# Performance work log

Measured on AMD Instinct MI355X. Metric: run time of the kernel, lower is better.

## Reference

```python
import jax, jax.numpy as jnp
import numpy as np

D = 1024


def setup_inputs() -> dict:
    key = jax.random.key(0)
    kx, kq, kk, kv, ko = jax.random.split(key, 5)
    scale = 0.02
    x = jax.random.normal(kx, (4, 2048, D), dtype=jnp.float32)
    Wq = jax.random.normal(kq, (D, D), dtype=jnp.float32) * scale
    Wk = jax.random.normal(kk, (D, D), dtype=jnp.float32) * scale
    Wv = jax.random.normal(kv, (D, D), dtype=jnp.float32) * scale
    Wo = jax.random.normal(ko, (D, D), dtype=jnp.float32) * scale
    return {"x": x, "Wq": Wq, "Wk": Wk, "Wv": Wv, "Wo": Wo}


def reference(x, Wq, Wk, Wv, Wo):
    # Linear projections (torch Linear: y = x @ W.T, no bias)
    q = jnp.einsum('bsd,ed->bse', x, Wq)
    k = jnp.einsum('bsd,ed->bse', x, Wk)
    v = jnp.einsum('bsd,ed->bse', x, Wv)
    d = x.shape[-1]
    # HRR binding: circular convolution of k and v along feature dim (rfft domain)
    Fk = jnp.fft.rfft(k, axis=-1)
    Fv = jnp.fft.rfft(v, axis=-1)
    Fq = jnp.fft.rfft(q, axis=-1)
    Fkv = Fk * Fv                      # bound key-value pairs, Fourier domain
    # causal cumulative memory over sequence; FFT is linear so cumsum commutes
    Fmem = jnp.cumsum(Fkv, axis=-2)    # [b, s, d//2+1] complex
    # unbind with query: circular correlation = multiply by conj(rfft(q))
    values_hat = jnp.fft.irfft(Fmem * jnp.conj(Fq), n=d, axis=-1)
    return jnp.einsum('bsd,ed->bse', values_hat, Wo)
```

## Files before the change

kernel.cpp:

```cpp
#include <hip/hip_runtime.h>

#define D_DIM 1024
#define NF 513
#define NB 4
#define NS 2048
#define NTOK (NB * NS)
#define NCH 32
#define CHS (NS / NCH)

typedef __attribute__((ext_vector_type(8))) short short8_t;
typedef __attribute__((ext_vector_type(4))) float f32x4;

__device__ inline unsigned short f2bf(float f) {
    unsigned u = __builtin_bit_cast(unsigned, f);
    u += 0x7FFFu + ((u >> 16) & 1u);
    return (unsigned short)(u >> 16);
}
__device__ inline float bf2f(unsigned short h) {
    unsigned u = ((unsigned)h) << 16;
    return __builtin_bit_cast(float, u);
}
__device__ inline unsigned pkc(float re, float im) {
    return (unsigned)f2bf(re) | ((unsigned)f2bf(im) << 16);
}
__device__ inline float2 upc(unsigned u) {
    return make_float2(bf2f((unsigned short)(u & 0xFFFFu)), bf2f((unsigned short)(u >> 16)));
}

__global__ __launch_bounds__(256) void convert_x(const float* __restrict__ src,
                                                 unsigned short* __restrict__ dst,
                                                 int n4) {
    int i = blockIdx.x * 256 + threadIdx.x;
    int stride = gridDim.x * 256;
    for (; i < n4; i += stride) {
        float4 v = reinterpret_cast<const float4*>(src)[i];
        ushort4 o;
        o.x = f2bf(v.x); o.y = f2bf(v.y); o.z = f2bf(v.z); o.w = f2bf(v.w);
        reinterpret_cast<ushort4*>(dst)[i] = o;
    }
}

__global__ __launch_bounds__(256) void convert_w(const float* __restrict__ Wq,
                                                 const float* __restrict__ Wk,
                                                 const float* __restrict__ Wv,
                                                 const float* __restrict__ Wo,
                                                 unsigned short* __restrict__ Wqkv,
                                                 unsigned short* __restrict__ Wob) {
    int y = blockIdx.y;
    const float* src = (y == 0) ? Wq : (y == 1) ? Wk : (y == 2) ? Wv : Wo;
    unsigned short* dst = (y < 3) ? (Wqkv + (size_t)y * 1048576) : Wob;
    int i = blockIdx.x * 256 + threadIdx.x;
    float4 v = reinterpret_cast<const float4*>(src)[i];
    ushort4 o;
    o.x = f2bf(v.x); o.y = f2bf(v.y); o.z = f2bf(v.z); o.w = f2bf(v.w);
    reinterpret_cast<ushort4*>(dst)[i] = o;
}

__device__ inline void gload_lds16(const void* g, void* l) {
    __builtin_amdgcn_global_load_lds(
        (const __attribute__((address_space(1))) void*)g,
        (__attribute__((address_space(3))) void*)l,
        16, 0, 0);
}

template <typename OutT>
__global__ __launch_bounds__(256) void gemm_bf16_bk64(const unsigned short* __restrict__ A,
                                                      const unsigned short* __restrict__ B,
                                                      OutT* __restrict__ C,
                                                      int M, int N, int K) {
    __shared__ __attribute__((aligned(16))) unsigned short ldsA[2 * 128 * 64];
    __shared__ __attribute__((aligned(16))) unsigned short ldsB[2 * 128 * 64];
    const int tid  = threadIdx.x;
    const int wave = tid >> 6;
    const int lane = tid & 63;
    const int l15  = lane & 15;
    const int q4   = (lane >> 4) & 3;
    const int h7   = l15 & 7;
    const int p0   = ((q4)     ^ h7) << 3;
    const int p1   = ((4 + q4) ^ h7) << 3;
    const int wm   = (wave >> 1) * 64;
    const int wn   = (wave & 1) * 64;
    const int bm   = blockIdx.x * 128;
    const int bn   = blockIdx.y * 128;
    const int srow = tid >> 3;
    const int scol = (((tid & 7) ^ ((tid >> 3) & 7)) << 3);
    const int NT   = K >> 6;

    const unsigned short* Asrc = A + (size_t)(bm + srow) * K + scol;
    const unsigned short* Bsrc = B + (size_t)(bn + srow) * K + scol;
    const size_t cstep = (size_t)32 * K;

    f32x4 acc[4][4];
#pragma unroll
    for (int i = 0; i < 4; ++i)
#pragma unroll
        for (int j = 0; j < 4; ++j)
            acc[i][j] = (f32x4){0.f, 0.f, 0.f, 0.f};

    auto STAGE = [&](int t, int b) {
        const int k0 = t << 6;
        unsigned short* la = &ldsA[b * 8192 + tid * 8];
        unsigned short* lb = &ldsB[b * 8192 + tid * 8];
        gload_lds16(Asrc + k0,             la);
        gload_lds16(Asrc + cstep + k0,     la + 2048);
        gload_lds16(Asrc + 2 * cstep + k0, la + 4096);
        gload_lds16(Asrc + 3 * cstep + k0, la + 6144);
        gload_lds16(Bsrc + k0,             lb);
        gload_lds16(Bsrc + cstep + k0,     lb + 2048);
        gload_lds16(Bsrc + 2 * cstep + k0, lb + 4096);
        gload_lds16(Bsrc + 3 * cstep + k0, lb + 6144);
    };

    STAGE(0, 0);

    for (int j = 0; j < NT; ++j) {
        const int buf = j & 1;
        if (j + 1 < NT) {
            STAGE(j + 1, buf ^ 1);
            asm volatile("s_waitcnt vmcnt(8)" ::: "memory");
        } else {
            asm volatile("s_waitcnt vmcnt(0)" ::: "memory");
        }
        __builtin_amdgcn_s_barrier();
        asm volatile("" ::: "memory");

        const unsigned short* la = &ldsA[buf * 8192];
        const unsigned short* lb = &ldsB[buf * 8192];

        {
            short8_t af[4], bfv[4];
#pragma unroll
            for (int mi = 0; mi < 4; ++mi)
                af[mi] = *reinterpret_cast<const short8_t*>(&la[(wm + mi * 16 + l15) * 64 + p0]);
#pragma unroll
            for (int ni = 0; ni < 4; ++ni)
                bfv[ni] = *reinterpret_cast<const short8_t*>(&lb[(wn + ni * 16 + l15) * 64 + p0]);
            __builtin_amdgcn_s_setprio(1);
#pragma unroll
            for (int mi = 0; mi < 4; ++mi)
#pragma unroll
                for (int ni = 0; ni < 4; ++ni)
                    acc[mi][ni] = __builtin_amdgcn_mfma_f32_16x16x32_bf16(af[mi], bfv[ni], acc[mi][ni], 0, 0, 0);
            __builtin_amdgcn_s_setprio(0);
        }
        {
            short8_t af[4], bfv[4];
#pragma unroll
            for (int mi = 0; mi < 4; ++mi)
                af[mi] = *reinterpret_cast<const short8_t*>(&la[(wm + mi * 16 + l15) * 64 + p1]);
#pragma unroll
            for (int ni = 0; ni < 4; ++ni)
                bfv[ni] = *reinterpret_cast<const short8_t*>(&lb[(wn + ni * 16 + l15) * 64 + p1]);
            __builtin_amdgcn_s_setprio(1);
#pragma unroll
            for (int mi = 0; mi < 4; ++mi)
#pragma unroll
                for (int ni = 0; ni < 4; ++ni)
                    acc[mi][ni] = __builtin_amdgcn_mfma_f32_16x16x32_bf16(af[mi], bfv[ni], acc[mi][ni], 0, 0, 0);
            __builtin_amdgcn_s_setprio(0);
        }

        __builtin_amdgcn_s_barrier();
        asm volatile("" ::: "memory");
    }

#pragma unroll
    for (int mi = 0; mi < 4; ++mi) {
        int rbase = bm + wm + mi * 16 + (lane >> 4) * 4;
#pragma unroll
        for (int ni = 0; ni < 4; ++ni) {
            int col = bn + wn + ni * 16 + l15;
#pragma unroll
            for (int j = 0; j < 4; ++j) {
                float v = acc[mi][ni][j];
                if constexpr (sizeof(OutT) == 4)
                    C[(size_t)(rbase + j) * N + col] = v;
                else
                    C[(size_t)(rbase + j) * N + col] = f2bf(v);
            }
        }
    }
}

__device__ inline int sw(int i) { return i ^ ((i >> 4) & 15); }

__device__ inline int dr4(int n) {
    return ((n & 3) << 8) | (((n >> 2) & 3) << 6) | (((n >> 4) & 3) << 4) |
           (((n >> 6) & 3) << 2) | ((n >> 8) & 3);
}

__device__ inline float2 cmul(float2 a, float2 b) {
    return make_float2(a.x * b.x - a.y * b.y, a.x * b.y + a.y * b.x);
}

__device__ inline void fft1024_r4(float2* X, const float2* tw, int t) {
#pragma unroll
    for (int s = 0; s < 5; ++s) {
        const int L = 1 << (2 * s);
        const int r = t & (L - 1);
        const int base = ((t >> (2 * s)) << (2 * s + 2)) + r;
        float2 A  = X[sw(base)];
        float2 Bv = X[sw(base + L)];
        float2 Cv = X[sw(base + 2 * L)];
        float2 Dv = X[sw(base + 3 * L)];
        if (s != 0) {
            const int step = 1024 >> (2 * s + 2);
            Bv = cmul(Bv, tw[sw(r * step)]);
            Cv = cmul(Cv, tw[sw(2 * r * step)]);
            Dv = cmul(Dv, tw[sw(3 * r * step)]);
        }
        float2 e0 = make_float2(A.x + Cv.x, A.y + Cv.y);
        float2 e1 = make_float2(A.x - Cv.x, A.y - Cv.y);
        float2 o0 = make_float2(Bv.x + Dv.x, Bv.y + Dv.y);
        float2 o1 = make_float2(Bv.x - Dv.x, Bv.y - Dv.y);
        X[sw(base)]         = make_float2(e0.x + o0.x, e0.y + o0.y);
        X[sw(base + L)]     = make_float2(e1.x + o1.y, e1.y - o1.x);
        X[sw(base + 2 * L)] = make_float2(e0.x - o0.x, e0.y - o0.y);
        X[sw(base + 3 * L)] = make_float2(e1.x - o1.y, e1.y + o1.x);
        __syncthreads();
    }
}

__global__ __launch_bounds__(256) void twiddle_init(float2* __restrict__ twg) {
    int k = blockIdx.x * 256 + threadIdx.x;
    if (k < 768) {
        float ang = -6.283185307179586f * (float)k / 1024.0f;
        float s, c;
        sincosf(ang, &s, &c);
        twg[sw(k)] = make_float2(c, s);
    }
}

__global__ __launch_bounds__(256) void hrr_fft_fwd(const unsigned short* __restrict__ QKV,
                                                   const float2* __restrict__ twg,
                                                   unsigned* __restrict__ Fkv,
                                                   unsigned* __restrict__ Fq) {
    __shared__ __attribute__((aligned(16))) float2 X[1024];
    __shared__ __attribute__((aligned(16))) float2 twL[768];
    const int tid = threadIdx.x;
    const int t0 = blockIdx.x * 2, t1 = t0 + 1;
    for (int i = tid; i < 384; i += 256)
        reinterpret_cast<float4*>(twL)[i] = reinterpret_cast<const float4*>(twg)[i];

#pragma unroll
    for (int which = 0; which < 2; ++which) {
        const int tok = which ? t1 : t0;
        const ushort4* Kr = (const ushort4*)(QKV + (size_t)tok * 3072 + 1024);
        const ushort4* Vr = (const ushort4*)(QKV + (size_t)tok * 3072 + 2048);
        ushort4 k4 = Kr[tid], v4 = Vr[tid];
        X[sw(dr4(4 * tid + 0))] = make_float2(bf2f(k4.x), bf2f(v4.x));
        X[sw(dr4(4 * tid + 1))] = make_float2(bf2f(k4.y), bf2f(v4.y));
        X[sw(dr4(4 * tid + 2))] = make_float2(bf2f(k4.z), bf2f(v4.z));
        X[sw(dr4(4 * tid + 3))] = make_float2(bf2f(k4.w), bf2f(v4.w));
        __syncthreads();
        fft1024_r4(X, twL, tid);
        for (int j = tid; j < NF; j += 256) {
            float2 Zj = X[sw(j)];
            float2 Zm = X[sw((1024 - j) & 1023)];
            float2 Fk = make_float2(0.5f * (Zj.x + Zm.x), 0.5f * (Zj.y - Zm.y));
            float2 Fv = make_float2(0.5f * (Zj.y + Zm.y), 0.5f * (Zm.x - Zj.x));
            float2 p = cmul(Fk, Fv);
            Fkv[(size_t)tok * NF + j] = pkc(p.x, p.y);
        }
        __syncthreads();
    }
    {
        const ushort4* Q0 = (const ushort4*)(QKV + (size_t)t0 * 3072);
        const ushort4* Q1 = (const ushort4*)(QKV + (size_t)t1 * 3072);
        ushort4 a4 = Q0[tid], b4 = Q1[tid];
        X[sw(dr4(4 * tid + 0))] = make_float2(bf2f(a4.x), bf2f(b4.x));
        X[sw(dr4(4 * tid + 1))] = make_float2(bf2f(a4.y), bf2f(b4.y));
        X[sw(dr4(4 * tid + 2))] = make_float2(bf2f(a4.z), bf2f(b4.z));
        X[sw(dr4(4 * tid + 3))] = make_float2(bf2f(a4.w), bf2f(b4.w));
        __syncthreads();
        fft1024_r4(X, twL, tid);
        for (int j = tid; j < NF; j += 256) {
            float2 Zj = X[sw(j)];
            float2 Zm = X[sw((1024 - j) & 1023)];
            Fq[(size_t)t0 * NF + j] = pkc(0.5f * (Zj.x + Zm.x), 0.5f * (Zj.y - Zm.y));
            Fq[(size_t)t1 * NF + j] = pkc(0.5f * (Zj.y + Zm.y), 0.5f * (Zm.x - Zj.x));
        }
    }
}

__global__ __launch_bounds__(256) void hrr_chunk_sum(const unsigned* __restrict__ Fkv,
                                                     float2* __restrict__ part) {
    int f = blockIdx.x * 256 + threadIdx.x;
    if (f >= NF) return;
    int ch = blockIdx.y, b = blockIdx.z;
    float sx = 0.f, sy = 0.f;
    size_t base = ((size_t)b * NS + (size_t)ch * CHS) * NF + f;
    for (int i = 0; i < CHS; ++i) {
        float2 t = upc(Fkv[base + (size_t)i * NF]);
        sx += t.x; sy += t.y;
    }
    part[(size_t)(b * NCH + ch) * NF + f] = make_float2(sx, sy);
}

__global__ __launch_bounds__(256) void hrr_scan_apply(unsigned* __restrict__ Fkv,
                                                      const unsigned* __restrict__ Fq,
                                                      const float2* __restrict__ part) {
    int f = blockIdx.x * 256 + threadIdx.x;
    if (f >= NF) return;
    int ch = blockIdx.y, b = blockIdx.z;
    float rx = 0.f, ry = 0.f;
    for (int c2 = 0; c2 < ch; ++c2) {
        float2 p = part[(size_t)(b * NCH + c2) * NF + f];
        rx += p.x; ry += p.y;
    }
    size_t base = ((size_t)b * NS + (size_t)ch * CHS) * NF + f;
    for (int i = 0; i < CHS; ++i) {
        size_t idx = base + (size_t)i * NF;
        float2 kv = upc(Fkv[idx]);
        rx += kv.x; ry += kv.y;
        float2 q = upc(Fq[idx]);
        Fkv[idx] = pkc(rx * q.x + ry * q.y, ry * q.x - rx * q.y);
    }
}

__global__ __launch_bounds__(256) void hrr_ifft(const unsigned* __restrict__ U,
                                                const float2* __restrict__ twg,
                                                unsigned short* __restrict__ vhat) {
    __shared__ __attribute__((aligned(16))) float2 X[1024];
    __shared__ __attribute__((aligned(16))) float2 twL[768];
    const int tid = threadIdx.x;
    const int t0 = blockIdx.x * 2, t1 = t0 + 1;
    for (int i = tid; i < 384; i += 256)
        reinterpret_cast<float4*>(twL)[i] = reinterpret_cast<const float4*>(twg)[i];
    const unsigned* U1 = U + (size_t)t0 * NF;
    const unsigned* U2 = U + (size_t)t1 * NF;
#pragma unroll
    for (int c = 0; c < 4; ++c) {
        int j = tid + (c << 8);
        float2 Cv;
        if (j <= 512) {
            float2 u1 = upc(U1[j]), u2 = upc(U2[j]);
            Cv = make_float2(u1.x - u2.y, -u1.y - u2.x);
        } else {
            int m = 1024 - j;
            float2 u1 = upc(U1[m]), u2 = upc(U2[m]);
            Cv = make_float2(u1.x + u2.y, u1.y - u2.x);
        }
        X[sw(dr4(j))] = Cv;
    }
    __syncthreads();
    fft1024_r4(X, twL, tid);
    const float invN = 1.0f / 1024.0f;
#pragma unroll
    for (int c = 0; c < 4; ++c) {
        int n = tid + (c << 8);
        float2 w = X[sw(n)];
        vhat[(size_t)t0 * D_DIM + n] = f2bf(w.x * invN);
        vhat[(size_t)t1 * D_DIM + n] = f2bf(-w.y * invN);
    }
}

extern "C" void kernel_launch(void* const* d_in, const int* in_sizes, int n_in,
                              void* d_out, int out_size, void* d_ws, size_t ws_size,
                              hipStream_t stream) {
    const float* x  = (const float*)d_in[0];
    const float* Wq = (const float*)d_in[1];
    const float* Wk = (const float*)d_in[2];
    const float* Wv = (const float*)d_in[3];
    const float* Wo = (const float*)d_in[4];
    float* out = (float*)d_out;

    char* ws = (char*)d_ws;
    unsigned short* QKVb = (unsigned short*)(ws + 0);
    unsigned*       Fkv  = (unsigned*)      (ws + 50331648);
    unsigned*       Fq   = (unsigned*)      (ws + 67141632);
    float2*         part = (float2*)        (ws + 83951616);
    float2*         twg  = (float2*)        (ws + 84476928);
    unsigned short* Wob  = (unsigned short*)(ws + 84483072);
    unsigned short* Wqkv = (unsigned short*)(ws + 86580224);
    unsigned short* xb   = (unsigned short*)(ws + 92871680);
    unsigned short* vhat = (unsigned short*)(ws + 109648896);

    convert_x<<<2048, 256, 0, stream>>>(x, xb, NTOK * D_DIM / 4);
    convert_w<<<dim3(1024, 4), 256, 0, stream>>>(Wq, Wk, Wv, Wo, Wqkv, Wob);
    twiddle_init<<<3, 256, 0, stream>>>(twg);

    dim3 gq(NTOK / 128, 3072 / 128);
    gemm_bf16_bk64<unsigned short><<<gq, 256, 0, stream>>>(xb, Wqkv, QKVb, NTOK, 3072, D_DIM);

    hrr_fft_fwd<<<NTOK / 2, 256, 0, stream>>>(QKVb, twg, Fkv, Fq);

    dim3 gs((NF + 255) / 256, NCH, NB);
    hrr_chunk_sum<<<gs, 256, 0, stream>>>(Fkv, part);
    hrr_scan_apply<<<gs, 256, 0, stream>>>(Fkv, Fq, part);

    hrr_ifft<<<NTOK / 2, 256, 0, stream>>>(Fkv, twg, vhat);

    dim3 go(NTOK / 128, D_DIM / 128);
    gemm_bf16_bk64<float><<<go, 256, 0, stream>>>(vhat, Wob, out, NTOK, D_DIM, D_DIM);
}
```

Baseline: 169.9 us.

## Load GEMM B operand directly into registers instead of staging through LDS

The bf16 GEMM no longer stages the weight (B) tile through shared memory. Each wave loads its B fragments straight from global memory into registers, double-buffered across k-steps, while A keeps the LDS double buffer. This halves LDS traffic and footprint, which may allow higher occupancy. In exchange, B is loaded redundantly by the two waves sharing a column, uses more VGPRs, and relies on hand-tuned vmcnt waits.

```diff
diff --git a/kernel.cpp b/kernel.cpp
--- a/kernel.cpp
+++ b/kernel.cpp
@@ -64,12 +64,11 @@
 }
 
 template <typename OutT>
-__global__ __launch_bounds__(256) void gemm_bf16_bk64(const unsigned short* __restrict__ A,
+__global__ __launch_bounds__(256) void gemm_bf16_breg(const unsigned short* __restrict__ A,
                                                       const unsigned short* __restrict__ B,
                                                       OutT* __restrict__ C,
                                                       int M, int N, int K) {
     __shared__ __attribute__((aligned(16))) unsigned short ldsA[2 * 128 * 64];
-    __shared__ __attribute__((aligned(16))) unsigned short ldsB[2 * 128 * 64];
     const int tid  = threadIdx.x;
     const int wave = tid >> 6;
     const int lane = tid & 63;
@@ -87,8 +86,8 @@
     const int NT   = K >> 6;
 
     const unsigned short* Asrc = A + (size_t)(bm + srow) * K + scol;
-    const unsigned short* Bsrc = B + (size_t)(bn + srow) * K + scol;
     const size_t cstep = (size_t)32 * K;
+    const unsigned short* Bsrc = B + (size_t)(bn + wn + l15) * K + q4 * 8;
 
     f32x4 acc[4][4];
 #pragma unroll
@@ -97,72 +96,71 @@
         for (int j = 0; j < 4; ++j)
             acc[i][j] = (f32x4){0.f, 0.f, 0.f, 0.f};
 
-    auto STAGE = [&](int t, int b) {
+    auto STAGE_A = [&](int t, int b) {
         const int k0 = t << 6;
         unsigned short* la = &ldsA[b * 8192 + tid * 8];
-        unsigned short* lb = &ldsB[b * 8192 + tid * 8];
         gload_lds16(Asrc + k0,             la);
         gload_lds16(Asrc + cstep + k0,     la + 2048);
         gload_lds16(Asrc + 2 * cstep + k0, la + 4096);
         gload_lds16(Asrc + 3 * cstep + k0, la + 6144);
-        gload_lds16(Bsrc + k0,             lb);
-        gload_lds16(Bsrc + cstep + k0,     lb + 2048);
-        gload_lds16(Bsrc + 2 * cstep + k0, lb + 4096);
-        gload_lds16(Bsrc + 3 * cstep + k0, lb + 6144);
     };
-
-    STAGE(0, 0);
-
-    for (int j = 0; j < NT; ++j) {
-        const int buf = j & 1;
-        if (j + 1 < NT) {
-            STAGE(j + 1, buf ^ 1);
-            asm volatile("s_waitcnt vmcnt(8)" ::: "memory");
-        } else {
-            asm volatile("s_waitcnt vmcnt(0)" ::: "memory");
-        }
-        __builtin_amdgcn_s_barrier();
-        asm volatile("" ::: "memory");
-
-        const unsigned short* la = &ldsA[buf * 8192];
-        const unsigned short* lb = &ldsB[buf * 8192];
-
-        {
-            short8_t af[4], bfv[4];
-#pragma unroll
-            for (int mi = 0; mi < 4; ++mi)
-                af[mi] = *reinterpret_cast<const short8_t*>(&la[(wm + mi * 16 + l15) * 64 + p0]);
-#pragma unroll
-            for (int ni = 0; ni < 4; ++ni)
-                bfv[ni] = *reinterpret_cast<const short8_t*>(&lb[(wn + ni * 16 + l15) * 64 + p0]);
-            __builtin_amdgcn_s_setprio(1);
-#pragma unroll
-            for (int mi = 0; mi < 4; ++mi)
-#pragma unroll
-                for (int ni = 0; ni < 4; ++ni)
-                    acc[mi][ni] = __builtin_amdgcn_mfma_f32_16x16x32_bf16(af[mi], bfv[ni], acc[mi][ni], 0, 0, 0);
-            __builtin_amdgcn_s_setprio(0);
-        }
-        {
-            short8_t af[4], bfv[4];
-#pragma unroll
-            for (int mi = 0; mi < 4; ++mi)
-                af[mi] = *reinterpret_cast<const short8_t*>(&la[(wm + mi * 16 + l15) * 64 + p1]);
-#pragma unroll
-            for (int ni = 0; ni < 4; ++ni)
-                bfv[ni] = *reinterpret_cast<const short8_t*>(&lb[(wn + ni * 16 + l15) * 64 + p1]);
-            __builtin_amdgcn_s_setprio(1);
-#pragma unroll
-            for (int mi = 0; mi < 4; ++mi)
-#pragma unroll
-                for (int ni = 0; ni < 4; ++ni)
-                    acc[mi][ni] = __builtin_amdgcn_mfma_f32_16x16x32_bf16(af[mi], bfv[ni], acc[mi][ni], 0, 0, 0);
-            __builtin_amdgcn_s_setprio(0);
-        }
-
-        __builtin_amdgcn_s_barrier();
-        asm volatile("" ::: "memory");
-    }
+    auto LOADB = [&](int t, short8_t (&bf)[2][4]) {
+#pragma unroll
+        for (int ni = 0; ni < 4; ++ni) {
+            const unsigned short* p = Bsrc + (size_t)ni * 16 * K + (t << 6);
+            bf[0][ni] = *reinterpret_cast<const short8_t*>(p);
+            bf[1][ni] = *reinterpret_cast<const short8_t*>(p + 32);
+        }
+    };
+
+    short8_t b0[2][4], b1[2][4];
+
+    STAGE_A(0, 0);
+    asm volatile("" ::: "memory");
+    LOADB(0, b0);
+    asm volatile("" ::: "memory");
+
+#define ROUND(J, BUF, BUSE, BNEXT)                                              \
+    {                                                                           \
+        const int j_ = (J);                                                     \
+        if (j_ + 1 < NT) STAGE_A(j_ + 1, (BUF) ^ 1);                            \
+        asm volatile("" ::: "memory");                                          \
+        if (j_ + 1 < NT) LOADB(j_ + 1, BNEXT);                                  \
+        if (j_ + 1 < NT) asm volatile("s_waitcnt vmcnt(20)" ::: "memory");      \
+        else             asm volatile("s_waitcnt vmcnt(8)"  ::: "memory");      \
+        __builtin_amdgcn_s_barrier();                                           \
+        asm volatile("" ::: "memory");                                          \
+        const unsigned short* la = &ldsA[(BUF) * 8192];                         \
+        short8_t af[4];                                                         \
+        _Pragma("unroll")                                                       \
+        for (int mi = 0; mi < 4; ++mi)                                          \
+            af[mi] = *reinterpret_cast<const short8_t*>(&la[(wm + mi * 16 + l15) * 64 + p0]); \
+        __builtin_amdgcn_s_setprio(1);                                          \
+        _Pragma("unroll")                                                       \
+        for (int mi = 0; mi < 4; ++mi)                                          \
+            _Pragma("unroll")                                                   \
+            for (int ni = 0; ni < 4; ++ni)                                      \
+                acc[mi][ni] = __builtin_amdgcn_mfma_f32_16x16x32_bf16(af[mi], BUSE[0][ni], acc[mi][ni], 0, 0, 0); \
+        __builtin_amdgcn_s_setprio(0);                                          \
+        _Pragma("unroll")                                                       \
+        for (int mi = 0; mi < 4; ++mi)                                          \
+            af[mi] = *reinterpret_cast<const short8_t*>(&la[(wm + mi * 16 + l15) * 64 + p1]); \
+        __builtin_amdgcn_s_setprio(1);                                          \
+        _Pragma("unroll")                                                       \
+        for (int mi = 0; mi < 4; ++mi)                                          \
+            _Pragma("unroll")                                                   \
+            for (int ni = 0; ni < 4; ++ni)                                      \
+                acc[mi][ni] = __builtin_amdgcn_mfma_f32_16x16x32_bf16(af[mi], BUSE[1][ni], acc[mi][ni], 0, 0, 0); \
+        __builtin_amdgcn_s_setprio(0);                                          \
+        __builtin_amdgcn_s_barrier();                                           \
+        asm volatile("" ::: "memory");                                          \
+    }
+
+    for (int jj = 0; jj < NT; jj += 2) {
+        ROUND(jj,     0, b0, b1)
+        ROUND(jj + 1, 1, b1, b0)
+    }
+#undef ROUND
 
 #pragma unroll
     for (int mi = 0; mi < 4; ++mi) {
@@ -381,7 +379,7 @@
     twiddle_init<<<3, 256, 0, stream>>>(twg);
 
     dim3 gq(NTOK / 128, 3072 / 128);
-    gemm_bf16_bk64<unsigned short><<<gq, 256, 0, stream>>>(xb, Wqkv, QKVb, NTOK, 3072, D_DIM);
+    gemm_bf16_breg<unsigned short><<<gq, 256, 0, stream>>>(xb, Wqkv, QKVb, NTOK, 3072, D_DIM);
 
     hrr_fft_fwd<<<NTOK / 2, 256, 0, stream>>>(QKVb, twg, Fkv, Fq);
 
@@ -392,5 +390,5 @@
     hrr_ifft<<<NTOK / 2, 256, 0, stream>>>(Fkv, twg, vhat);
 
     dim3 go(NTOK / 128, D_DIM / 128);
-    gemm_bf16_bk64<float><<<go, 256, 0, stream>>>(vhat, Wob, out, NTOK, D_DIM, D_DIM);
-}
+    gemm_bf16_breg<float><<<go, 256, 0, stream>>>(vhat, Wob, out, NTOK, D_DIM, D_DIM);
+}
```

Measured after the change: 237.2 us. 39.6% more time.

## Fold rfft into projection weights and irfft into output weights

Applied to the files above, without the earlier changes.

The DFT is folded into the weight matrices: Wq/Wk/Wv are pre-transformed along the feature dim so the QKV GEMM directly produces rfft coefficients (fp16 output), and Wo absorbs the inverse real FFT, so the output GEMM consumes the unbound spectrum directly. This removes the per-token forward and inverse FFT kernels and the bf16 QKV/vhat intermediates, at the cost of a slightly wider first GEMM (3200 columns) and a K=1088 second GEMM. The k*v product is now recomputed inside the chunk-sum and scan kernels. Per-call weight FFT preprocessing adds work, and storing the spectra in fp16 and bf16 changes numerical accuracy.

```diff
diff --git a/kernel.cpp b/kernel.cpp
--- a/kernel.cpp
+++ b/kernel.cpp
@@ -1,4 +1,5 @@
 #include <hip/hip_runtime.h>
+#include <hip/hip_fp16.h>
 
 #define D_DIM 1024
 #define NF 513
@@ -7,6 +8,9 @@
 #define NTOK (NB * NS)
 #define NCH 32
 #define CHS (NS / NCH)
+#define NQKV 3200
+#define KOUT 1088
+#define USTRIDE 544
 
 typedef __attribute__((ext_vector_type(8))) short short8_t;
 typedef __attribute__((ext_vector_type(4))) float f32x4;
@@ -23,8 +27,10 @@
 __device__ inline unsigned pkc(float re, float im) {
     return (unsigned)f2bf(re) | ((unsigned)f2bf(im) << 16);
 }
-__device__ inline float2 upc(unsigned u) {
-    return make_float2(bf2f((unsigned short)(u & 0xFFFFu)), bf2f((unsigned short)(u >> 16)));
+__device__ inline float2 uph(unsigned u) {
+    unsigned short lo = (unsigned short)(u & 0xFFFFu), hi = (unsigned short)(u >> 16);
+    return make_float2(__half2float(__builtin_bit_cast(__half, lo)),
+                       __half2float(__builtin_bit_cast(__half, hi)));
 }
 
 __global__ __launch_bounds__(256) void convert_x(const float* __restrict__ src,
@@ -40,22 +46,6 @@
     }
 }
 
-__global__ __launch_bounds__(256) void convert_w(const float* __restrict__ Wq,
-                                                 const float* __restrict__ Wk,
-                                                 const float* __restrict__ Wv,
-                                                 const float* __restrict__ Wo,
-                                                 unsigned short* __restrict__ Wqkv,
-                                                 unsigned short* __restrict__ Wob) {
-    int y = blockIdx.y;
-    const float* src = (y == 0) ? Wq : (y == 1) ? Wk : (y == 2) ? Wv : Wo;
-    unsigned short* dst = (y < 3) ? (Wqkv + (size_t)y * 1048576) : Wob;
-    int i = blockIdx.x * 256 + threadIdx.x;
-    float4 v = reinterpret_cast<const float4*>(src)[i];
-    ushort4 o;
-    o.x = f2bf(v.x); o.y = f2bf(v.y); o.z = f2bf(v.z); o.w = f2bf(v.w);
-    reinterpret_cast<ushort4*>(dst)[i] = o;
-}
-
 __device__ inline void gload_lds16(const void* g, void* l) {
     __builtin_amdgcn_global_load_lds(
         (const __attribute__((address_space(1))) void*)g,
@@ -63,7 +53,7 @@
         16, 0, 0);
 }
 
-template <typename OutT>
+template <typename OutT, bool F16OUT>
 __global__ __launch_bounds__(256) void gemm_bf16_bk64(const unsigned short* __restrict__ A,
                                                       const unsigned short* __restrict__ B,
                                                       OutT* __restrict__ C,
@@ -175,6 +165,9 @@
                 float v = acc[mi][ni][j];
                 if constexpr (sizeof(OutT) == 4)
                     C[(size_t)(rbase + j) * N + col] = v;
+                else if constexpr (F16OUT)
+                    C[(size_t)(rbase + j) * N + col] =
+                        __builtin_bit_cast(unsigned short, __float2half(v));
                 else
                     C[(size_t)(rbase + j) * N + col] = f2bf(v);
             }
@@ -231,127 +224,118 @@
     }
 }
 
-__global__ __launch_bounds__(256) void hrr_fft_fwd(const unsigned short* __restrict__ QKV,
-                                                   const float2* __restrict__ twg,
-                                                   unsigned* __restrict__ Fkv,
-                                                   unsigned* __restrict__ Fq) {
+__global__ __launch_bounds__(256) void wf_qkv(const float* __restrict__ Wq,
+                                              const float* __restrict__ Wk,
+                                              const float* __restrict__ Wv,
+                                              const float2* __restrict__ twg,
+                                              unsigned short* __restrict__ WF) {
     __shared__ __attribute__((aligned(16))) float2 X[1024];
     __shared__ __attribute__((aligned(16))) float2 twL[768];
     const int tid = threadIdx.x;
-    const int t0 = blockIdx.x * 2, t1 = t0 + 1;
+    const int w = blockIdx.y;
+    const float* W = (w == 0) ? Wq : (w == 1) ? Wk : Wv;
+    const int d0 = blockIdx.x * 2;
     for (int i = tid; i < 384; i += 256)
         reinterpret_cast<float4*>(twL)[i] = reinterpret_cast<const float4*>(twg)[i];
-
-#pragma unroll
-    for (int which = 0; which < 2; ++which) {
-        const int tok = which ? t1 : t0;
-        const ushort4* Kr = (const ushort4*)(QKV + (size_t)tok * 3072 + 1024);
-        const ushort4* Vr = (const ushort4*)(QKV + (size_t)tok * 3072 + 2048);
-        ushort4 k4 = Kr[tid], v4 = Vr[tid];
-        X[sw(dr4(4 * tid + 0))] = make_float2(bf2f(k4.x), bf2f(v4.x));
-        X[sw(dr4(4 * tid + 1))] = make_float2(bf2f(k4.y), bf2f(v4.y));
-        X[sw(dr4(4 * tid + 2))] = make_float2(bf2f(k4.z), bf2f(v4.z));
-        X[sw(dr4(4 * tid + 3))] = make_float2(bf2f(k4.w), bf2f(v4.w));
-        __syncthreads();
-        fft1024_r4(X, twL, tid);
-        for (int j = tid; j < NF; j += 256) {
-            float2 Zj = X[sw(j)];
-            float2 Zm = X[sw((1024 - j) & 1023)];
-            float2 Fk = make_float2(0.5f * (Zj.x + Zm.x), 0.5f * (Zj.y - Zm.y));
-            float2 Fv = make_float2(0.5f * (Zj.y + Zm.y), 0.5f * (Zm.x - Zj.x));
-            float2 p = cmul(Fk, Fv);
-            Fkv[(size_t)tok * NF + j] = pkc(p.x, p.y);
-        }
-        __syncthreads();
-    }
-    {
-        const ushort4* Q0 = (const ushort4*)(QKV + (size_t)t0 * 3072);
-        const ushort4* Q1 = (const ushort4*)(QKV + (size_t)t1 * 3072);
-        ushort4 a4 = Q0[tid], b4 = Q1[tid];
-        X[sw(dr4(4 * tid + 0))] = make_float2(bf2f(a4.x), bf2f(b4.x));
-        X[sw(dr4(4 * tid + 1))] = make_float2(bf2f(a4.y), bf2f(b4.y));
-        X[sw(dr4(4 * tid + 2))] = make_float2(bf2f(a4.z), bf2f(b4.z));
-        X[sw(dr4(4 * tid + 3))] = make_float2(bf2f(a4.w), bf2f(b4.w));
-        __syncthreads();
-        fft1024_r4(X, twL, tid);
-        for (int j = tid; j < NF; j += 256) {
-            float2 Zj = X[sw(j)];
-            float2 Zm = X[sw((1024 - j) & 1023)];
-            Fq[(size_t)t0 * NF + j] = pkc(0.5f * (Zj.x + Zm.x), 0.5f * (Zj.y - Zm.y));
-            Fq[(size_t)t1 * NF + j] = pkc(0.5f * (Zj.y + Zm.y), 0.5f * (Zm.x - Zj.x));
-        }
-    }
-}
-
-__global__ __launch_bounds__(256) void hrr_chunk_sum(const unsigned* __restrict__ Fkv,
+    for (int n = tid; n < 1024; n += 256) {
+        float2 z = *reinterpret_cast<const float2*>(W + (size_t)n * 1024 + d0);
+        X[sw(dr4(n))] = z;
+    }
+    __syncthreads();
+    fft1024_r4(X, twL, tid);
+    const int rbase = w * 1026;
+    for (int f = tid; f < NF; f += 256) {
+        float2 Zj = X[sw(f)];
+        float2 Zm = X[sw((1024 - f) & 1023)];
+        float re0 = 0.5f * (Zj.x + Zm.x), im0 = 0.5f * (Zj.y - Zm.y);
+        float re1 = 0.5f * (Zj.y + Zm.y), im1 = 0.5f * (Zm.x - Zj.x);
+        WF[(size_t)(rbase + 2 * f)     * 1024 + d0]     = f2bf(re0);
+        WF[(size_t)(rbase + 2 * f + 1) * 1024 + d0]     = f2bf(im0);
+        WF[(size_t)(rbase + 2 * f)     * 1024 + d0 + 1] = f2bf(re1);
+        WF[(size_t)(rbase + 2 * f + 1) * 1024 + d0 + 1] = f2bf(im1);
+    }
+}
+
+__global__ __launch_bounds__(256) void wf_zero(unsigned* __restrict__ p) {
+    int i = blockIdx.x * 256 + threadIdx.x;
+    if (i < 62464) p[i] = 0;
+}
+
+__global__ __launch_bounds__(256) void wf_o(const float* __restrict__ Wo,
+                                            const float2* __restrict__ twg,
+                                            unsigned short* __restrict__ Wt) {
+    __shared__ __attribute__((aligned(16))) float2 X[1024];
+    __shared__ __attribute__((aligned(16))) float2 twL[768];
+    const int tid = threadIdx.x;
+    const int e0 = blockIdx.x * 2;
+    for (int i = tid; i < 384; i += 256)
+        reinterpret_cast<float4*>(twL)[i] = reinterpret_cast<const float4*>(twg)[i];
+    const float* r0 = Wo + (size_t)e0 * 1024;
+    const float* r1 = r0 + 1024;
+    for (int n = tid; n < 1024; n += 256)
+        X[sw(dr4(n))] = make_float2(r0[n], r1[n]);
+    __syncthreads();
+    fft1024_r4(X, twL, tid);
+    unsigned short* o0 = Wt + (size_t)e0 * KOUT;
+    unsigned short* o1 = o0 + KOUT;
+    for (int f = tid; f < NF; f += 256) {
+        float2 Zj = X[sw(f)];
+        float2 Zm = X[sw((1024 - f) & 1023)];
+        float c = (f == 0 || f == 512) ? (1.0f / 1024.0f) : (2.0f / 1024.0f);
+        o0[2 * f]     = f2bf(0.5f * (Zj.x + Zm.x) * c);
+        o0[2 * f + 1] = f2bf(0.5f * (Zj.y - Zm.y) * c);
+        o1[2 * f]     = f2bf(0.5f * (Zj.y + Zm.y) * c);
+        o1[2 * f + 1] = f2bf(0.5f * (Zm.x - Zj.x) * c);
+    }
+    for (int j = tid; j < KOUT - 2 * NF; j += 256) {
+        o0[2 * NF + j] = 0;
+        o1[2 * NF + j] = 0;
+    }
+}
+
+__global__ __launch_bounds__(256) void hrr_chunk_sum(const unsigned* __restrict__ F,
                                                      float2* __restrict__ part) {
     int f = blockIdx.x * 256 + threadIdx.x;
     if (f >= NF) return;
     int ch = blockIdx.y, b = blockIdx.z;
     float sx = 0.f, sy = 0.f;
-    size_t base = ((size_t)b * NS + (size_t)ch * CHS) * NF + f;
+    size_t base = ((size_t)b * NS + (size_t)ch * CHS) * 1600;
     for (int i = 0; i < CHS; ++i) {
-        float2 t = upc(Fkv[base + (size_t)i * NF]);
-        sx += t.x; sy += t.y;
+        size_t row = base + (size_t)i * 1600;
+        float2 k = uph(F[row + 513 + f]);
+        float2 v = uph(F[row + 1026 + f]);
+        sx += k.x * v.x - k.y * v.y;
+        sy += k.x * v.y + k.y * v.x;
     }
     part[(size_t)(b * NCH + ch) * NF + f] = make_float2(sx, sy);
 }
 
-__global__ __launch_bounds__(256) void hrr_scan_apply(unsigned* __restrict__ Fkv,
-                                                      const unsigned* __restrict__ Fq,
-                                                      const float2* __restrict__ part) {
+__global__ __launch_bounds__(256) void hrr_scan_apply(const unsigned* __restrict__ F,
+                                                      const float2* __restrict__ part,
+                                                      unsigned* __restrict__ U) {
     int f = blockIdx.x * 256 + threadIdx.x;
-    if (f >= NF) return;
+    if (f >= USTRIDE) return;
     int ch = blockIdx.y, b = blockIdx.z;
+    size_t ubase = ((size_t)b * NS + (size_t)ch * CHS) * USTRIDE + f;
+    if (f >= NF) {
+        for (int i = 0; i < CHS; ++i) U[ubase + (size_t)i * USTRIDE] = 0;
+        return;
+    }
     float rx = 0.f, ry = 0.f;
     for (int c2 = 0; c2 < ch; ++c2) {
         float2 p = part[(size_t)(b * NCH + c2) * NF + f];
         rx += p.x; ry += p.y;
     }
-    size_t base = ((size_t)b * NS + (size_t)ch * CHS) * NF + f;
+    size_t base = ((size_t)b * NS + (size_t)ch * CHS) * 1600;
     for (int i = 0; i < CHS; ++i) {
-        size_t idx = base + (size_t)i * NF;
-        float2 kv = upc(Fkv[idx]);
-        rx += kv.x; ry += kv.y;
-        float2 q = upc(Fq[idx]);
-        Fkv[idx] = pkc(rx * q.x + ry * q.y, ry * q.x - rx * q.y);
-    }
-}
-
-__global__ __launch_bounds__(256) void hrr_ifft(const unsigned* __restrict__ U,
-                                                const float2* __restrict__ twg,
-                                                unsigned short* __restrict__ vhat) {
-    __shared__ __attribute__((aligned(16))) float2 X[1024];
-    __shared__ __attribute__((aligned(16))) float2 twL[768];
-    const int tid = threadIdx.x;
-    const int t0 = blockIdx.x * 2, t1 = t0 + 1;
-    for (int i = tid; i < 384; i += 256)
-        reinterpret_cast<float4*>(twL)[i] = reinterpret_cast<const float4*>(twg)[i];
-    const unsigned* U1 = U + (size_t)t0 * NF;
-    const unsigned* U2 = U + (size_t)t1 * NF;
-#pragma unroll
-    for (int c = 0; c < 4; ++c) {
-        int j = tid + (c << 8);
-        float2 Cv;
-        if (j <= 512) {
-            float2 u1 = upc(U1[j]), u2 = upc(U2[j]);
-            Cv = make_float2(u1.x - u2.y, -u1.y - u2.x);
-        } else {
-            int m = 1024 - j;
-            float2 u1 = upc(U1[m]), u2 = upc(U2[m]);
-            Cv = make_float2(u1.x + u2.y, u1.y - u2.x);
-        }
-        X[sw(dr4(j))] = Cv;
-    }
-    __syncthreads();
-    fft1024_r4(X, twL, tid);
-    const float invN = 1.0f / 1024.0f;
-#pragma unroll
-    for (int c = 0; c < 4; ++c) {
-        int n = tid + (c << 8);
-        float2 w = X[sw(n)];
-        vhat[(size_t)t0 * D_DIM + n] = f2bf(w.x * invN);
-        vhat[(size_t)t1 * D_DIM + n] = f2bf(-w.y * invN);
+        size_t row = base + (size_t)i * 1600;
+        float2 k = uph(F[row + 513 + f]);
+        float2 v = uph(F[row + 1026 + f]);
+        rx += k.x * v.x - k.y * v.y;
+        ry += k.x * v.y + k.y * v.x;
+        float2 q = uph(F[row + f]);
+        U[ubase + (size_t)i * USTRIDE] = pkc(rx * q.x + ry * q.y,
+                                            ry * q.x - rx * q.y);
     }
 }
 
@@ -366,31 +350,28 @@
     float* out = (float*)d_out;
 
     char* ws = (char*)d_ws;
-    unsigned short* QKVb = (unsigned short*)(ws + 0);
-    unsigned*       Fkv  = (unsigned*)      (ws + 50331648);
-    unsigned*       Fq   = (unsigned*)      (ws + 67141632);
-    float2*         part = (float2*)        (ws + 83951616);
-    float2*         twg  = (float2*)        (ws + 84476928);
-    unsigned short* Wob  = (unsigned short*)(ws + 84483072);
-    unsigned short* Wqkv = (unsigned short*)(ws + 86580224);
-    unsigned short* xb   = (unsigned short*)(ws + 92871680);
-    unsigned short* vhat = (unsigned short*)(ws + 109648896);
+    unsigned short* F_all = (unsigned short*)(ws + 0);
+    unsigned short* U     = (unsigned short*)(ws + 52428800);
+    float2*         part  = (float2*)        (ws + 70254592);
+    float2*         twg   = (float2*)        (ws + 70779904);
+    unsigned short* WF    = (unsigned short*)(ws + 70786048);
+    unsigned short* Wt    = (unsigned short*)(ws + 77339648);
+    unsigned short* xb    = (unsigned short*)(ws + 79567872);
 
     convert_x<<<2048, 256, 0, stream>>>(x, xb, NTOK * D_DIM / 4);
-    convert_w<<<dim3(1024, 4), 256, 0, stream>>>(Wq, Wk, Wv, Wo, Wqkv, Wob);
     twiddle_init<<<3, 256, 0, stream>>>(twg);
 
-    dim3 gq(NTOK / 128, 3072 / 128);
-    gemm_bf16_bk64<unsigned short><<<gq, 256, 0, stream>>>(xb, Wqkv, QKVb, NTOK, 3072, D_DIM);
-
-    hrr_fft_fwd<<<NTOK / 2, 256, 0, stream>>>(QKVb, twg, Fkv, Fq);
-
-    dim3 gs((NF + 255) / 256, NCH, NB);
-    hrr_chunk_sum<<<gs, 256, 0, stream>>>(Fkv, part);
-    hrr_scan_apply<<<gs, 256, 0, stream>>>(Fkv, Fq, part);
-
-    hrr_ifft<<<NTOK / 2, 256, 0, stream>>>(Fkv, twg, vhat);
+    wf_qkv<<<dim3(512, 3), 256, 0, stream>>>(Wq, Wk, Wv, twg, WF);
+    wf_zero<<<244, 256, 0, stream>>>((unsigned*)(WF + (size_t)3078 * 1024));
+    wf_o<<<512, 256, 0, stream>>>(Wo, twg, Wt);
+
+    dim3 gq(NTOK / 128, NQKV / 128);
+    gemm_bf16_bk64<unsigned short, true><<<gq, 256, 0, stream>>>(xb, WF, F_all, NTOK, NQKV, D_DIM);
+
+    dim3 gs((USTRIDE + 255) / 256, NCH, NB);
+    hrr_chunk_sum<<<dim3(3, NCH, NB), 256, 0, stream>>>((const unsigned*)F_all, part);
+    hrr_scan_apply<<<gs, 256, 0, stream>>>((const unsigned*)F_all, part, (unsigned*)U);
 
     dim3 go(NTOK / 128, D_DIM / 128);
-    gemm_bf16_bk64<float><<<go, 256, 0, stream>>>(vhat, Wob, out, NTOK, D_DIM, D_DIM);
-}
+    gemm_bf16_bk64<float, false><<<go, 256, 0, stream>>>(U, Wt, out, NTOK, D_DIM, KOUT);
+}
```

Result: slower. 191.3 us (+12.6%).
